# Kernel optimization log

Measured on AMD Instinct MI355X. Metric: run time of the kernel, lower is better.

Reference implementation:

```python
import jax, jax.numpy as jnp
import numpy as np

EPS = 1e-12  # tf.nn.l2_normalize epsilon used by keras Dot(normalize=True)

def setup_inputs() -> dict:
    key = jax.random.key(0)
    k1, k2 = jax.random.split(key)
    a = jax.random.normal(k1, (16, 4096, 256), dtype=jnp.float32)
    b = jax.random.normal(k2, (16, 4096, 256), dtype=jnp.float32)
    return {"a": a, "b": b}

def _l2_normalize(x, axis=-1):
    # matches tf.nn.l2_normalize: x * rsqrt(max(sum(x^2), eps))
    sq = jnp.sum(x * x, axis=axis, keepdims=True)
    return x * jax.lax.rsqrt(jnp.maximum(sq, EPS))

def reference(a, b):
    # Original: full [B,N,N] cosine-similarity matrix then diag_part.
    # The diagonal equals the rowwise cosine similarity, computed directly.
    an = _l2_normalize(a, axis=2)  # [B, N, D]
    bn = _l2_normalize(b, axis=2)  # [B, N, D]
    return jnp.sum(an * bn, axis=2)  # [B, N]
```

## Files before the change

kernel.cpp:

```cpp
#include <hip/hip_runtime.h>


#define D          256
#define D4         64
#define EPS        1e-12f
#define LANES_ROW  8
#define ROWS_WAVE  8
#define F4_LANE    8
#define WAVES_BLK  4

__global__ __launch_bounds__(256) void cosine_rows_kernel(
    const float* __restrict__ a,
    const float* __restrict__ b,
    float* __restrict__ out,
    int n_rows)
{
    const int lane = threadIdx.x & 63;
    const int wave = threadIdx.x >> 6;
    const int g    = lane >> 3;
    const int s    = lane & 7;

    const int row = (blockIdx.x * WAVES_BLK + wave) * ROWS_WAVE + g;
    if (row >= n_rows) return;

    const float4* a4 = reinterpret_cast<const float4*>(a) + (size_t)row * D4 + s;
    const float4* b4 = reinterpret_cast<const float4*>(b) + (size_t)row * D4 + s;

    float4 av[F4_LANE], bv[F4_LANE];
    #pragma unroll
    for (int k = 0; k < F4_LANE; ++k) {
        av[k] = a4[k * LANES_ROW];
        bv[k] = b4[k * LANES_ROW];
    }

    float sa = 0.f, sb = 0.f, sab = 0.f;
    #pragma unroll
    for (int k = 0; k < F4_LANE; ++k) {
        sa  += av[k].x * av[k].x + av[k].y * av[k].y + av[k].z * av[k].z + av[k].w * av[k].w;
        sb  += bv[k].x * bv[k].x + bv[k].y * bv[k].y + bv[k].z * bv[k].z + bv[k].w * bv[k].w;
        sab += av[k].x * bv[k].x + av[k].y * bv[k].y + av[k].z * bv[k].z + av[k].w * bv[k].w;
    }

    #pragma unroll
    for (int off = 1; off < LANES_ROW; off <<= 1) {
        sa  += __shfl_xor(sa,  off, 64);
        sb  += __shfl_xor(sb,  off, 64);
        sab += __shfl_xor(sab, off, 64);
    }

    if (s == 0) {
        out[row] = sab * rsqrtf(fmaxf(sa, EPS)) * rsqrtf(fmaxf(sb, EPS));
    }
}

extern "C" void kernel_launch(void* const* d_in, const int* in_sizes, int n_in,
                              void* d_out, int out_size, void* d_ws, size_t ws_size,
                              hipStream_t stream)
{
    const float* a = (const float*)d_in[0];
    const float* b = (const float*)d_in[1];
    float* out = (float*)d_out;

    const int n_rows = out_size;
    const int rows_per_block = WAVES_BLK * ROWS_WAVE;
    const int grid = (n_rows + rows_per_block - 1) / rows_per_block;

    cosine_rows_kernel<<<grid, 256, 0, stream>>>(a, b, out, n_rows);
}
```

Measured before the change: 142.6 us.

## Double-buffer row chunks per wave with 16 lanes per row

```diff
diff --git a/kernel.cpp b/kernel.cpp
--- a/kernel.cpp
+++ b/kernel.cpp
@@ -1,12 +1,13 @@
 #include <hip/hip_runtime.h>
 
 
-#define D          256
 #define D4         64
 #define EPS        1e-12f
-#define LANES_ROW  8
-#define ROWS_WAVE  8
-#define F4_LANE    8
+#define LANES_ROW  16
+#define CHUNK_ROWS 4
+#define F4_CHUNK   4
+#define NCHUNK     4
+#define ROWS_WAVE  (CHUNK_ROWS * NCHUNK)
 #define WAVES_BLK  4
 
 __global__ __launch_bounds__(256) void cosine_rows_kernel(
@@ -17,39 +18,58 @@
 {
     const int lane = threadIdx.x & 63;
     const int wave = threadIdx.x >> 6;
-    const int g    = lane >> 3;
-    const int s    = lane & 7;
+    const int g    = lane >> 4;
+    const int s    = lane & 15;
 
-    const int row = (blockIdx.x * WAVES_BLK + wave) * ROWS_WAVE + g;
-    if (row >= n_rows) return;
+    const int wave_id = blockIdx.x * WAVES_BLK + wave;
+    const int row0    = wave_id * ROWS_WAVE;
+    if (row0 >= n_rows) return;
 
-    const float4* a4 = reinterpret_cast<const float4*>(a) + (size_t)row * D4 + s;
-    const float4* b4 = reinterpret_cast<const float4*>(b) + (size_t)row * D4 + s;
+    const float4* A = reinterpret_cast<const float4*>(a) + (size_t)(row0 + g) * D4 + s;
+    const float4* B = reinterpret_cast<const float4*>(b) + (size_t)(row0 + g) * D4 + s;
 
-    float4 av[F4_LANE], bv[F4_LANE];
+    float4 av[2][F4_CHUNK], bv[2][F4_CHUNK];
+
     #pragma unroll
-    for (int k = 0; k < F4_LANE; ++k) {
-        av[k] = a4[k * LANES_ROW];
-        bv[k] = b4[k * LANES_ROW];
-    }
-
-    float sa = 0.f, sb = 0.f, sab = 0.f;
-    #pragma unroll
-    for (int k = 0; k < F4_LANE; ++k) {
-        sa  += av[k].x * av[k].x + av[k].y * av[k].y + av[k].z * av[k].z + av[k].w * av[k].w;
-        sb  += bv[k].x * bv[k].x + bv[k].y * bv[k].y + bv[k].z * bv[k].z + bv[k].w * bv[k].w;
-        sab += av[k].x * bv[k].x + av[k].y * bv[k].y + av[k].z * bv[k].z + av[k].w * bv[k].w;
+    for (int k = 0; k < F4_CHUNK; ++k) {
+        av[0][k] = A[k * LANES_ROW];
+        bv[0][k] = B[k * LANES_ROW];
     }
 
     #pragma unroll
-    for (int off = 1; off < LANES_ROW; off <<= 1) {
-        sa  += __shfl_xor(sa,  off, 64);
-        sb  += __shfl_xor(sb,  off, 64);
-        sab += __shfl_xor(sab, off, 64);
-    }
+    for (int c = 0; c < NCHUNK; ++c) {
+        const int cur = c & 1;
+        const int nxt = cur ^ 1;
 
-    if (s == 0) {
-        out[row] = sab * rsqrtf(fmaxf(sa, EPS)) * rsqrtf(fmaxf(sb, EPS));
+        if (c < NCHUNK - 1) {
+            #pragma unroll
+            for (int k = 0; k < F4_CHUNK; ++k) {
+                av[nxt][k] = A[(c + 1) * CHUNK_ROWS * D4 + k * LANES_ROW];
+                bv[nxt][k] = B[(c + 1) * CHUNK_ROWS * D4 + k * LANES_ROW];
+            }
+        }
+
+        float sa = 0.f, sb = 0.f, sab = 0.f;
+        #pragma unroll
+        for (int k = 0; k < F4_CHUNK; ++k) {
+            float4 x = av[cur][k], y = bv[cur][k];
+            sa  += x.x * x.x + x.y * x.y + x.z * x.z + x.w * x.w;
+            sb  += y.x * y.x + y.y * y.y + y.z * y.z + y.w * y.w;
+            sab += x.x * y.x + x.y * y.y + x.z * y.z + x.w * y.w;
+        }
+
+        #pragma unroll
+        for (int off = 1; off < LANES_ROW; off <<= 1) {
+            sa  += __shfl_xor(sa,  off, 64);
+            sb  += __shfl_xor(sb,  off, 64);
+            sab += __shfl_xor(sab, off, 64);
+        }
+
+        if (s == 0) {
+            const int r = row0 + c * CHUNK_ROWS + g;
+            if (r < n_rows)
+                out[r] = sab * rsqrtf(fmaxf(sa, EPS)) * rsqrtf(fmaxf(sb, EPS));
+        }
     }
 }
 
```

After: 144.6 us. Within noise of the previous version (+1.4%).
